# Performance work log

Measured on AMD Instinct MI355X. Metric: run time of the kernel, lower is better.

## Reference

```python
import jax, jax.numpy as jnp
import numpy as np

WS = 6        # window size -> N = 36 tokens per window
HEADS = 16

def _rel_index(ws):
    coords = np.stack(np.meshgrid(np.arange(ws), np.arange(ws), indexing='ij')).reshape(2, -1)
    rel = coords[:, :, None] - coords[:, None, :] + (ws - 1)
    return jnp.asarray(rel[0] * (2 * ws - 1) + rel[1])  # (N, N) int

REL_IDX = _rel_index(WS)

def _ln(x, g, b, eps=1e-5):
    m = x.mean(-1, keepdims=True)
    v = x.var(-1, keepdims=True)
    return (x - m) / jnp.sqrt(v + eps) * g + b

def setup_inputs() -> dict:
    key = jax.random.key(0)
    ks = jax.random.split(key, 6)
    B, H, W, C = 16, 96, 96, 512
    hid = 4 * C
    s = 0.02
    return {
        'x': jax.random.normal(ks[0], (B, H, W, C), jnp.float32),
        'w_qkv': jax.random.normal(ks[1], (C, 3 * C), jnp.float32) * s,
        'w_proj': jax.random.normal(ks[2], (C, C), jnp.float32) * s,
        'b_proj': jnp.zeros((C,), jnp.float32),
        'rel_bias': jax.random.normal(ks[3], ((2 * WS - 1) ** 2, HEADS), jnp.float32) * s,
        'ln1_g': jnp.ones((C,), jnp.float32), 'ln1_b': jnp.zeros((C,), jnp.float32),
        'ln2_g': jnp.ones((C,), jnp.float32), 'ln2_b': jnp.zeros((C,), jnp.float32),
        'w_fc1': jax.random.normal(ks[4], (C, hid), jnp.float32) * s,
        'b_fc1': jnp.zeros((hid,), jnp.float32),
        'w_fc2': jax.random.normal(ks[5], (hid, C), jnp.float32) * s,
        'b_fc2': jnp.zeros((C,), jnp.float32),
    }

def reference(x, w_qkv, w_proj, b_proj, rel_bias, ln1_g, ln1_b, ln2_g, ln2_b, w_fc1, b_fc1, w_fc2, b_fc2):
    B, H, W, C = x.shape
    h, d, N = HEADS, C // HEADS, WS * WS
    nh, nw = H // WS, W // WS
    # window partition: (B,H,W,C) -> (B*nh*nw, N, C)
    xw = x.reshape(B, nh, WS, nw, WS, C).transpose(0, 1, 3, 2, 4, 5).reshape(B * nh * nw, N, C)
    xn = _ln(xw, ln1_g, ln1_b)
    qkv = xn @ w_qkv
    q, k, v = jnp.split(qkv, 3, axis=-1)
    to_heads = lambda t: t.reshape(-1, N, h, d).transpose(0, 2, 1, 3)  # (B_, h, N, d)
    q = to_heads(q) * (d ** -0.5)
    k = to_heads(k)
    v = to_heads(v)
    attn = jnp.einsum('bhnd,bhmd->bhnm', q, k)
    bias = rel_bias[REL_IDX.reshape(-1)].reshape(N, N, h).transpose(2, 0, 1)  # (h, N, N)
    attn = jax.nn.softmax(attn + bias[None], axis=-1)
    o = jnp.einsum('bhnm,bhmd->bhnd', attn, v).transpose(0, 2, 1, 3).reshape(-1, N, C)
    o = o @ w_proj + b_proj
    # un-window; NOTE: source has no residual around attention (x is replaced)
    x2 = o.reshape(B, nh, nw, WS, WS, C).transpose(0, 1, 3, 2, 4, 5).reshape(B, H, W, C)
    xm = _ln(x2, ln2_g, ln2_b)
    mlp = jax.nn.gelu(xm @ w_fc1 + b_fc1, approximate=False) @ w_fc2 + b_fc2
    return x2 + mlp
```

## Files before the change

kernel.cpp:

```cpp
#include <hip/hip_runtime.h>
#include <stdint.h>

#define TOK 147456
#define CCH 512

typedef __attribute__((ext_vector_type(8))) short short8;
typedef __attribute__((ext_vector_type(4))) float f32x4;

struct alignas(8) US4 { unsigned short a, b, c, d; };

typedef __attribute__((address_space(3))) void lds_void;
typedef const __attribute__((address_space(1))) void gbl_void;

__device__ inline void gload16(const void* g, void* l) {
    __builtin_amdgcn_global_load_lds((gbl_void*)g, (lds_void*)l, 16, 0, 0);
}

__device__ inline unsigned short f2bf(float f) {
    union { float f; unsigned u; } v{f};
    unsigned r = v.u + 0x7fffu + ((v.u >> 16) & 1u);
    return (unsigned short)(r >> 16);
}
__device__ inline float bf2f(unsigned short h) {
    union { unsigned u; float f; } v; v.u = ((unsigned)h) << 16; return v.f;
}
__device__ inline float frcp(float x) {
    float r; asm("v_rcp_f32 %0, %1" : "=v"(r) : "v"(x)); return r;
}

__global__ void wprep(const float* __restrict__ in, unsigned short* __restrict__ out,
                      int K, int N) {
    int idx = blockIdx.x * 256 + threadIdx.x;
    if (idx >= K * N) return;
    int k = idx / N, n = idx % N;
    out[(size_t)n * K + k] = f2bf(in[idx]);
}

__global__ void biasprep(const float* __restrict__ rb, float* __restrict__ bb) {
    int idx = blockIdx.x * 256 + threadIdx.x;
    if (idx >= 16 * 48 * 48) return;
    int h = idx / 2304, rem = idx % 2304, r = rem / 48, c = rem % 48;
    float v = -1e9f;
    if (r < 36 && c < 36) {
        int dy = r / 6 - c / 6 + 5;
        int dx = r % 6 - c % 6 + 5;
        v = rb[(dy * 11 + dx) * 16 + h];
    }
    bb[idx] = v;
}

__global__ __launch_bounds__(256) void ln_k(const float* __restrict__ x,
                                            const float* __restrict__ g,
                                            const float* __restrict__ b,
                                            unsigned short* __restrict__ out, int ntok) {
    int lane = threadIdx.x & 63;
    int tok = blockIdx.x * 4 + (threadIdx.x >> 6);
    if (tok >= ntok) return;
    const float4* xr = (const float4*)(x + (size_t)tok * CCH);
    float4 v0 = xr[lane], v1 = xr[lane + 64];
    float s  = v0.x + v0.y + v0.z + v0.w + v1.x + v1.y + v1.z + v1.w;
    float s2 = v0.x*v0.x + v0.y*v0.y + v0.z*v0.z + v0.w*v0.w
             + v1.x*v1.x + v1.y*v1.y + v1.z*v1.z + v1.w*v1.w;
#pragma unroll
    for (int off = 32; off; off >>= 1) { s += __shfl_xor(s, off); s2 += __shfl_xor(s2, off); }
    float mean = s * (1.f / 512.f);
    float var  = s2 * (1.f / 512.f) - mean * mean;
    float inv  = rsqrtf(var + 1e-5f);
    const float4* gp = (const float4*)g;
    const float4* bp = (const float4*)b;
    float4 g0 = gp[lane], g1 = gp[lane + 64], b0 = bp[lane], b1 = bp[lane + 64];
    US4 o0, o1;
    o0.a = f2bf((v0.x - mean) * inv * g0.x + b0.x);
    o0.b = f2bf((v0.y - mean) * inv * g0.y + b0.y);
    o0.c = f2bf((v0.z - mean) * inv * g0.z + b0.z);
    o0.d = f2bf((v0.w - mean) * inv * g0.w + b0.w);
    o1.a = f2bf((v1.x - mean) * inv * g1.x + b1.x);
    o1.b = f2bf((v1.y - mean) * inv * g1.y + b1.y);
    o1.c = f2bf((v1.z - mean) * inv * g1.z + b1.z);
    o1.d = f2bf((v1.w - mean) * inv * g1.w + b1.w);
    unsigned short* op = out + (size_t)tok * CCH;
    *(US4*)(op + 4 * lane)       = o0;
    *(US4*)(op + 256 + 4 * lane) = o1;
}

__global__ __launch_bounds__(256) void ln_bf(const unsigned short* __restrict__ x,
                                             const float* __restrict__ g,
                                             const float* __restrict__ b,
                                             unsigned short* __restrict__ out, int ntok) {
    int lane = threadIdx.x & 63;
    int tok = blockIdx.x * 4 + (threadIdx.x >> 6);
    if (tok >= ntok) return;
    short8 v = *(const short8*)(x + (size_t)tok * CCH + lane * 8);
    float f[8];
#pragma unroll
    for (int j = 0; j < 8; ++j) f[j] = bf2f((unsigned short)v[j]);
    float s = 0.f, s2 = 0.f;
#pragma unroll
    for (int j = 0; j < 8; ++j) { s += f[j]; s2 += f[j] * f[j]; }
#pragma unroll
    for (int off = 32; off; off >>= 1) { s += __shfl_xor(s, off); s2 += __shfl_xor(s2, off); }
    float mean = s * (1.f / 512.f);
    float var  = s2 * (1.f / 512.f) - mean * mean;
    float inv  = rsqrtf(var + 1e-5f);
    const float4* gp = (const float4*)g + lane * 2;
    const float4* bp = (const float4*)b + lane * 2;
    float4 g0 = gp[0], g1 = gp[1], b0 = bp[0], b1 = bp[1];
    float gg[8] = {g0.x, g0.y, g0.z, g0.w, g1.x, g1.y, g1.z, g1.w};
    float bb[8] = {b0.x, b0.y, b0.z, b0.w, b1.x, b1.y, b1.z, b1.w};
    short8 o;
#pragma unroll
    for (int j = 0; j < 8; ++j) o[j] = (short)f2bf((f[j] - mean) * inv * gg[j] + bb[j]);
    *(short8*)(out + (size_t)tok * CCH + lane * 8) = o;
}

__global__ __launch_bounds__(256) void attn_mfma(const unsigned short* __restrict__ qkv,
                                                 const float* __restrict__ biasb,
                                                 unsigned short* __restrict__ o) {
    __shared__ __align__(16) unsigned short p_lds[4][48 * 64];
    __shared__ __align__(16) unsigned short v_lds[4][32 * 64];

    int tid  = threadIdx.x;
    int wv   = tid >> 6;
    int lane = tid & 63;
    int l15  = lane & 15;
    int g    = lane >> 4;

    int wid = blockIdx.x * 4 + wv;
    int h   = wid & 15;
    int win = wid >> 4;
    int img  = win >> 8;
    int wrow = (win >> 4) & 15;
    int wcol = win & 15;
    int tok_base = (img * 96 + wrow * 6) * 96 + wcol * 6;

    unsigned short* pw = p_lds[wv];
    unsigned short* vw = v_lds[wv];

    #define TOKOF(r) (tok_base + (r) + 90 * ((r) / 6))

    short8 z8 = {};
    for (int e = lane; e < 224; e += 64) {
        if (e < 128) {
            int ch = e >> 2, kst = 32 + (e & 3) * 8;
            *(short8*)(vw + ch * 64 + (kst ^ ((ch & 7) << 3))) = z8;
        } else {
            int ee = e - 128; int q = ee >> 1, kst = 48 + (ee & 1) * 8;
            *(short8*)(pw + q * 64 + (kst ^ ((q & 7) << 3))) = z8;
        }
    }

    for (int e = lane; e < 144; e += 64) {
        int r = e >> 2, c0 = (e & 3) * 8;
        short8 vv = *(const short8*)(qkv + (size_t)TOKOF(r) * 1536 + 1024 + h * 32 + c0);
#pragma unroll
        for (int j = 0; j < 8; ++j) {
            int ch = c0 + j;
            vw[ch * 64 + (r ^ ((ch & 7) << 3))] = (unsigned short)vv[j];
        }
    }

    short8 qf[3], kf[3];
#pragma unroll
    for (int t = 0; t < 3; ++t) {
        int r = t * 16 + l15;
        if (r < 36) {
            size_t ba = (size_t)TOKOF(r) * 1536 + h * 32 + g * 8;
            qf[t] = *(const short8*)(qkv + ba);
            kf[t] = *(const short8*)(qkv + ba + 512);
        } else { qf[t] = z8; kf[t] = z8; }
    }

    f32x4 s[3][3] = {};
#pragma unroll
    for (int mt = 0; mt < 3; ++mt)
#pragma unroll
        for (int nt = 0; nt < 3; ++nt)
            s[mt][nt] = __builtin_amdgcn_mfma_f32_16x16x32_bf16(qf[mt], kf[nt], s[mt][nt], 0, 0, 0);

    const float SCALE = 0.17677669529663687f;
    const float* bh = biasb + h * 2304;
#pragma unroll
    for (int mt = 0; mt < 3; ++mt) {
#pragma unroll
        for (int r = 0; r < 4; ++r) {
            int row = mt * 16 + g * 4 + r;
            const float* bb = bh + row * 48 + l15;
            float v0 = fmaf(s[mt][0][r], SCALE, bb[0]);
            float v1 = fmaf(s[mt][1][r], SCALE, bb[16]);
            float v2 = fmaf(s[mt][2][r], SCALE, bb[32]);
            float m = fmaxf(fmaxf(v0, v1), v2);
#pragma unroll
            for (int off = 1; off < 16; off <<= 1) m = fmaxf(m, __shfl_xor(m, off));
            float e0 = __expf(v0 - m), e1 = __expf(v1 - m), e2 = __expf(v2 - m);
            float sm = e0 + e1 + e2;
#pragma unroll
            for (int off = 1; off < 16; off <<= 1) sm += __shfl_xor(sm, off);
            float inv = 1.f / sm;
            int sw = (row & 7) << 3;
            unsigned short* pr = pw + row * 64;
            pr[(l15)      ^ sw] = f2bf(e0 * inv);
            pr[(16 + l15) ^ sw] = f2bf(e1 * inv);
            pr[(32 + l15) ^ sw] = f2bf(e2 * inv);
        }
    }

    f32x4 oacc[3][2] = {};
#pragma unroll
    for (int ks = 0; ks < 2; ++ks) {
        int kst = ks * 32 + g * 8;
        short8 bfr[2];
#pragma unroll
        for (int nt = 0; nt < 2; ++nt) {
            int c = nt * 16 + l15;
            bfr[nt] = *(const short8*)(vw + c * 64 + (kst ^ ((c & 7) << 3)));
        }
#pragma unroll
        for (int mt = 0; mt < 3; ++mt) {
            int q = mt * 16 + l15;
            short8 pa = *(const short8*)(pw + q * 64 + (kst ^ ((q & 7) << 3)));
#pragma unroll
            for (int nt = 0; nt < 2; ++nt)
                oacc[mt][nt] = __builtin_amdgcn_mfma_f32_16x16x32_bf16(pa, bfr[nt], oacc[mt][nt], 0, 0, 0);
        }
    }

#pragma unroll
    for (int mt = 0; mt < 3; ++mt) {
#pragma unroll
        for (int r = 0; r < 4; ++r) {
            int q = mt * 16 + g * 4 + r;
            if (q < 36) {
                size_t rb = (size_t)TOKOF(q) * 512 + h * 32;
#pragma unroll
                for (int nt = 0; nt < 2; ++nt)
                    o[rb + nt * 16 + l15] = f2bf(oacc[mt][nt][r]);
            }
        }
    }
    #undef TOKOF
}

template <int EPI>
__global__ __launch_bounds__(512, 1) void gemm8(const unsigned short* __restrict__ A,
                                                const unsigned short* __restrict__ Bt,
                                                int M, int N, int K,
                                                const float* __restrict__ bias,
                                                const unsigned short* __restrict__ resid,
                                                void* __restrict__ Cout) {
    extern __shared__ char lds[];
    int tid = threadIdx.x;
    int w = tid >> 6, lane = tid & 63;
    int l15 = lane & 15, grp = lane >> 4, l7 = l15 & 7;
    int wm = w >> 2, wn = w & 3;

    int nbn = N >> 8;
    int nwg = gridDim.x;
    int q = nwg >> 3, r = nwg & 7;
    int xcd = blockIdx.x & 7, pos_ = blockIdx.x >> 3;
    int wgid = (xcd < r ? xcd * (q + 1) : r * (q + 1) + (xcd - r) * q) + pos_;
    int bm = wgid / nbn, bn = wgid % nbn;

    int NI = K >> 7;

    int trow = tid >> 3;
    int sg = (tid & 7) ^ (trow & 7);
    const unsigned short* aBase = A  + ((size_t)bm * 256 + trow) * (size_t)K + sg * 8;
    const unsigned short* bBase = Bt + ((size_t)bn * 256 + trow) * (size_t)K + sg * 8;

    #define STG(base, rowOff, kt, dst) do { \
        gload16((base) + (size_t)(rowOff) * K + (kt),        lds + (dst) + tid * 16); \
        gload16((base) + (size_t)((rowOff) + 64) * K + (kt), lds + (dst) + 8192 + tid * 16); } while (0)

    int aR0 = wm * 16384 + l15 * 128 + ((grp ^ l7) << 4);
    int bR0 = 32768 + (wn >> 1) * 16384 + (wn & 1) * 8192 + l15 * 128 + ((grp ^ l7) << 4);

    f32x4 acc[8][4] = {};
    short8 Af[4][2], Bf[4][2];

    STG(bBase, 0,   0,  32768);
    STG(bBase, 128, 0,  32768 + 16384);
    STG(aBase, 0,   0,  0);
    STG(aBase, 128, 0,  16384);
    STG(bBase, 0,   64, 65536 + 32768);
    STG(bBase, 128, 64, 65536 + 32768 + 16384);
    asm volatile("s_waitcnt vmcnt(4)" ::: "memory");
    __builtin_amdgcn_s_barrier();

    #define RDA(d, qm) do { int ab_ = (d) * 65536 + (qm) * 8192 + aR0; \
        _Pragma("unroll") for (int mi_ = 0; mi_ < 4; ++mi_) { \
            Af[mi_][0] = *(const short8*)(lds + ab_ + mi_ * 2048); \
            Af[mi_][1] = *(const short8*)(lds + ((ab_ + mi_ * 2048) ^ 64)); } } while (0)
    #define RDB(d, nh) do { int bb_ = (d) * 65536 + (nh) * 4096 + bR0; \
        _Pragma("unroll") for (int nj_ = 0; nj_ < 2; ++nj_) { \
            Bf[(nh) * 2 + nj_][0] = *(const short8*)(lds + bb_ + nj_ * 2048); \
            Bf[(nh) * 2 + nj_][1] = *(const short8*)(lds + ((bb_ + nj_ * 2048) ^ 64)); } } while (0)
    #define MFQ(qm, nh) do { \
        _Pragma("unroll") for (int mi_ = 0; mi_ < 4; ++mi_) \
        _Pragma("unroll") for (int nj_ = 0; nj_ < 2; ++nj_) \
        _Pragma("unroll") for (int ks_ = 0; ks_ < 2; ++ks_) \
            acc[(qm) * 4 + mi_][(nh) * 2 + nj_] = __builtin_amdgcn_mfma_f32_16x16x32_bf16( \
                Af[mi_][ks_], Bf[(nh) * 2 + nj_][ks_], acc[(qm) * 4 + mi_][(nh) * 2 + nj_], 0, 0, 0); } while (0)
    #define PH_PRE  do { __builtin_amdgcn_s_barrier(); \
        asm volatile("s_waitcnt lgkmcnt(0)" ::: "memory"); \
        __builtin_amdgcn_sched_barrier(0); \
        __builtin_amdgcn_s_setprio(1); } while (0)
    #define PH_POST do { __builtin_amdgcn_s_setprio(0); \
        __builtin_amdgcn_s_barrier(); } while (0)

    for (int i = 0; i < NI; ++i) {
        int tka = i << 7, tkb = tka + 64;
        bool pf = (i + 1 < NI);
        RDA(0, 0); RDB(0, 0);
        STG(aBase, 0, tkb, 65536);
        PH_PRE; MFQ(0, 0); PH_POST;
        RDB(0, 1);
        STG(aBase, 128, tkb, 65536 + 16384);
        PH_PRE; MFQ(0, 1); PH_POST;
        RDA(0, 1);
        if (pf) STG(bBase, 0, tka + 128, 32768);
        PH_PRE; MFQ(1, 0); PH_POST;
        if (pf) {
            STG(bBase, 128, tka + 128, 32768 + 16384);
            asm volatile("s_waitcnt vmcnt(4)" ::: "memory");
        } else {
            asm volatile("s_waitcnt vmcnt(0)" ::: "memory");
        }
        PH_PRE; MFQ(1, 1); PH_POST;
        RDA(1, 0); RDB(1, 0);
        if (pf) STG(aBase, 0, tka + 128, 0);
        PH_PRE; MFQ(0, 0); PH_POST;
        RDB(1, 1);
        if (pf) STG(aBase, 128, tka + 128, 16384);
        PH_PRE; MFQ(0, 1); PH_POST;
        RDA(1, 1);
        if (pf) STG(bBase, 0, tkb + 128, 65536 + 32768);
        PH_PRE; MFQ(1, 0); PH_POST;
        if (pf) {
            STG(bBase, 128, tkb + 128, 65536 + 32768 + 16384);
            asm volatile("s_waitcnt vmcnt(4)" ::: "memory");
        }
        PH_PRE; MFQ(1, 1); PH_POST;
    }
    #undef STG
    #undef RDA
    #undef RDB
    #undef MFQ
    #undef PH_PRE
    #undef PH_POST

    int row0 = bm * 256 + wm * 128 + grp * 4;
    int col0 = bn * 256 + wn * 64 + l15;
#pragma unroll
    for (int m = 0; m < 8; ++m) {
#pragma unroll
        for (int n = 0; n < 4; ++n) {
            int col = col0 + n * 16;
            float bv = (EPI == 0) ? 0.f : bias[col];
#pragma unroll
            for (int r2 = 0; r2 < 4; ++r2) {
                int row = row0 + m * 16 + r2;
                size_t idx = (size_t)row * N + col;
                float val = acc[m][n][r2] + bv;
                if (EPI == 0) {
                    ((unsigned short*)Cout)[idx] = f2bf(val);
                } else if (EPI == 1) {
                    ((unsigned short*)Cout)[idx] = f2bf(val);
                } else if (EPI == 2) {
                    float t1 = val * val;
                    float t2 = fmaf(t1, 0.0713548163f, 1.5957691216f);
                    float z  = val * t2;
                    float e  = __expf(z);
                    float rr = frcp(e + 1.f);
                    float ge = val - val * rr;
                    ((unsigned short*)Cout)[idx] = f2bf(ge);
                } else {
                    ((float*)Cout)[idx] = val + bf2f(resid[idx]);
                }
            }
        }
    }
}

extern "C" void kernel_launch(void* const* d_in, const int* in_sizes, int n_in,
                              void* d_out, int out_size, void* d_ws, size_t ws_size,
                              hipStream_t stream) {
    const float* x       = (const float*)d_in[0];
    const float* w_qkv   = (const float*)d_in[1];
    const float* w_proj  = (const float*)d_in[2];
    const float* b_proj  = (const float*)d_in[3];
    const float* relb    = (const float*)d_in[4];
    const float* ln1g    = (const float*)d_in[5];
    const float* ln1b    = (const float*)d_in[6];
    const float* ln2g    = (const float*)d_in[7];
    const float* ln2b    = (const float*)d_in[8];
    const float* w_fc1   = (const float*)d_in[9];
    const float* b_fc1   = (const float*)d_in[10];
    const float* w_fc2   = (const float*)d_in[11];
    const float* b_fc2   = (const float*)d_in[12];
    float* out = (float*)d_out;

    hipFuncSetAttribute(reinterpret_cast<const void*>(&gemm8<0>),
                        hipFuncAttributeMaxDynamicSharedMemorySize, 131072);
    hipFuncSetAttribute(reinterpret_cast<const void*>(&gemm8<1>),
                        hipFuncAttributeMaxDynamicSharedMemorySize, 131072);
    hipFuncSetAttribute(reinterpret_cast<const void*>(&gemm8<2>),
                        hipFuncAttributeMaxDynamicSharedMemorySize, 131072);
    hipFuncSetAttribute(reinterpret_cast<const void*>(&gemm8<3>),
                        hipFuncAttributeMaxDynamicSharedMemorySize, 131072);

    char* w = (char*)d_ws;
    unsigned short* wT_qkv  = (unsigned short*)w; w += (size_t)1536 * 512 * 2;
    unsigned short* wT_proj = (unsigned short*)w; w += (size_t)512  * 512 * 2;
    unsigned short* wT_fc1  = (unsigned short*)w; w += (size_t)2048 * 512 * 2;
    unsigned short* wT_fc2  = (unsigned short*)w; w += (size_t)512  * 2048 * 2;
    float* biasb            = (float*)w;          w += (size_t)16 * 48 * 48 * 4;
    size_t wbytes = (size_t)(w - (char*)d_ws);

    int nchunk = 16;
    for (int c = 1; c <= 16; c *= 2) {
        size_t tokc = TOK / c;
        if (wbytes + tokc * 6144 <= ws_size) { nchunk = c; break; }
    }
    size_t tokc = TOK / nchunk;
    unsigned short* buf1 = (unsigned short*)w;
    unsigned short* buf2 = (unsigned short*)(w + tokc * 1024);
    unsigned short* buf3 = (unsigned short*)(w + tokc * 5120);

    wprep<<<(512 * 1536 + 255) / 256, 256, 0, stream>>>(w_qkv,  wT_qkv,  512, 1536);
    wprep<<<(512 * 512  + 255) / 256, 256, 0, stream>>>(w_proj, wT_proj, 512, 512);
    wprep<<<(512 * 2048 + 255) / 256, 256, 0, stream>>>(w_fc1,  wT_fc1,  512, 2048);
    wprep<<<(2048 * 512 + 255) / 256, 256, 0, stream>>>(w_fc2,  wT_fc2,  2048, 512);
    biasprep<<<(16 * 48 * 48 + 255) / 256, 256, 0, stream>>>(relb, biasb);

    int Mc = (int)tokc;
    int gm = Mc / 256;
    int imgs = Mc / 9216;

    for (int c = 0; c < nchunk; ++c) {
        size_t toff = (size_t)c * tokc;
        const float* xc = x + toff * CCH;
        float* outc = out + toff * CCH;

        ln_k<<<Mc / 4, 256, 0, stream>>>(xc, ln1g, ln1b, buf1, Mc);
        gemm8<0><<<gm * 6, 512, 131072, stream>>>(buf1, wT_qkv, Mc, 1536, 512,
                                                  nullptr, nullptr, buf2);
        attn_mfma<<<imgs * 1024, 256, 0, stream>>>(buf2, biasb, buf1);
        gemm8<1><<<gm * 2, 512, 131072, stream>>>(buf1, wT_proj, Mc, 512, 512,
                                                  b_proj, nullptr, buf3);
        ln_bf<<<Mc / 4, 256, 0, stream>>>(buf3, ln2g, ln2b, buf1, Mc);
        gemm8<2><<<gm * 8, 512, 131072, stream>>>(buf1, wT_fc1, Mc, 2048, 512,
                                                  b_fc1, nullptr, buf2);
        gemm8<3><<<gm * 2, 512, 131072, stream>>>(buf2, wT_fc2, Mc, 512, 2048,
                                                  b_fc2, buf3, outc);
    }
}
```

Before: 1.508 ms.

## Make GEMM persistent with cross-tile prefetch and vectorized transposed epilogue

The GEMM becomes a persistent kernel with a fixed grid of 256 workgroups. Each workgroup loops over output tiles using the XCD-aware tile mapping and prefetches the next tile's first K-slices during the last K iteration of the current tile. The goal is to hide the pipeline prologue and tail between tiles and to avoid wave quantization. The MFMA operands are swapped so each lane holds four consecutive columns, which lets the epilogue write 4-wide vector stores and load bias and residual as vectors. The risks are more register pressure and the epilogue still serializing against the next tile's compute.

Result: slower. 1.590 ms (+5.5%).

```diff
diff --git a/kernel.cpp b/kernel.cpp
--- a/kernel.cpp
+++ b/kernel.cpp
@@ -254,18 +254,17 @@
     int wm = w >> 2, wn = w & 3;
 
     int nbn = N >> 8;
+    int ntiles = (M >> 8) * nbn;
+    int NI = K >> 7;
     int nwg = gridDim.x;
-    int q = nwg >> 3, r = nwg & 7;
-    int xcd = blockIdx.x & 7, pos_ = blockIdx.x >> 3;
-    int wgid = (xcd < r ? xcd * (q + 1) : r * (q + 1) + (xcd - r) * q) + pos_;
-    int bm = wgid / nbn, bn = wgid % nbn;
-
-    int NI = K >> 7;
+
+    int tq = ntiles >> 3, tr = ntiles & 7;
+    #define TMAP(t, bmv, bnv) do { int x_ = (t) & 7, p_ = (t) >> 3; \
+        int wg_ = (x_ < tr ? x_ * (tq + 1) : tr * (tq + 1) + (x_ - tr) * tq) + p_; \
+        bmv = wg_ / nbn; bnv = wg_ % nbn; } while (0)
 
     int trow = tid >> 3;
     int sg = (tid & 7) ^ (trow & 7);
-    const unsigned short* aBase = A  + ((size_t)bm * 256 + trow) * (size_t)K + sg * 8;
-    const unsigned short* bBase = Bt + ((size_t)bn * 256 + trow) * (size_t)K + sg * 8;
 
     #define STG(base, rowOff, kt, dst) do { \
         gload16((base) + (size_t)(rowOff) * K + (kt),        lds + (dst) + tid * 16); \
@@ -276,6 +275,11 @@
 
     f32x4 acc[8][4] = {};
     short8 Af[4][2], Bf[4][2];
+
+    int traw = blockIdx.x;
+    int bm, bn; TMAP(traw, bm, bn);
+    const unsigned short* aBase = A  + ((size_t)bm * 256 + trow) * (size_t)K + sg * 8;
+    const unsigned short* bBase = Bt + ((size_t)bn * 256 + trow) * (size_t)K + sg * 8;
 
     STG(bBase, 0,   0,  32768);
     STG(bBase, 128, 0,  32768 + 16384);
@@ -299,7 +303,7 @@
         _Pragma("unroll") for (int nj_ = 0; nj_ < 2; ++nj_) \
         _Pragma("unroll") for (int ks_ = 0; ks_ < 2; ++ks_) \
             acc[(qm) * 4 + mi_][(nh) * 2 + nj_] = __builtin_amdgcn_mfma_f32_16x16x32_bf16( \
-                Af[mi_][ks_], Bf[(nh) * 2 + nj_][ks_], acc[(qm) * 4 + mi_][(nh) * 2 + nj_], 0, 0, 0); } while (0)
+                Bf[(nh) * 2 + nj_][ks_], Af[mi_][ks_], acc[(qm) * 4 + mi_][(nh) * 2 + nj_], 0, 0, 0); } while (0)
     #define PH_PRE  do { __builtin_amdgcn_s_barrier(); \
         asm volatile("s_waitcnt lgkmcnt(0)" ::: "memory"); \
         __builtin_amdgcn_sched_barrier(0); \
@@ -307,39 +311,106 @@
     #define PH_POST do { __builtin_amdgcn_s_setprio(0); \
         __builtin_amdgcn_s_barrier(); } while (0)
 
-    for (int i = 0; i < NI; ++i) {
-        int tka = i << 7, tkb = tka + 64;
-        bool pf = (i + 1 < NI);
-        RDA(0, 0); RDB(0, 0);
-        STG(aBase, 0, tkb, 65536);
-        PH_PRE; MFQ(0, 0); PH_POST;
-        RDB(0, 1);
-        STG(aBase, 128, tkb, 65536 + 16384);
-        PH_PRE; MFQ(0, 1); PH_POST;
-        RDA(0, 1);
-        if (pf) STG(bBase, 0, tka + 128, 32768);
-        PH_PRE; MFQ(1, 0); PH_POST;
-        if (pf) {
-            STG(bBase, 128, tka + 128, 32768 + 16384);
-            asm volatile("s_waitcnt vmcnt(4)" ::: "memory");
-        } else {
-            asm volatile("s_waitcnt vmcnt(0)" ::: "memory");
-        }
-        PH_PRE; MFQ(1, 1); PH_POST;
-        RDA(1, 0); RDB(1, 0);
-        if (pf) STG(aBase, 0, tka + 128, 0);
-        PH_PRE; MFQ(0, 0); PH_POST;
-        RDB(1, 1);
-        if (pf) STG(aBase, 128, tka + 128, 16384);
-        PH_PRE; MFQ(0, 1); PH_POST;
-        RDA(1, 1);
-        if (pf) STG(bBase, 0, tkb + 128, 65536 + 32768);
-        PH_PRE; MFQ(1, 0); PH_POST;
-        if (pf) {
-            STG(bBase, 128, tkb + 128, 65536 + 32768 + 16384);
-            asm volatile("s_waitcnt vmcnt(4)" ::: "memory");
-        }
-        PH_PRE; MFQ(1, 1); PH_POST;
+    while (true) {
+        int tnext = traw + nwg;
+        bool hasNext = tnext < ntiles;
+        const unsigned short* aNB = aBase;
+        const unsigned short* bNB = bBase;
+        if (hasNext) {
+            int bm2, bn2; TMAP(tnext, bm2, bn2);
+            aNB = A  + ((size_t)bm2 * 256 + trow) * (size_t)K + sg * 8;
+            bNB = Bt + ((size_t)bn2 * 256 + trow) * (size_t)K + sg * 8;
+        }
+        for (int i = 0; i < NI; ++i) {
+            int tka = i << 7, tkb = tka + 64;
+            bool lastI = (i + 1 == NI);
+            const unsigned short* aS = lastI ? aNB : aBase;
+            const unsigned short* bS = lastI ? bNB : bBase;
+            int ktN = lastI ? 0 : (tka + 128);
+            bool pf = (!lastI) || hasNext;
+            RDA(0, 0); RDB(0, 0);
+            STG(aBase, 0, tkb, 65536);
+            PH_PRE; MFQ(0, 0); PH_POST;
+            RDB(0, 1);
+            STG(aBase, 128, tkb, 65536 + 16384);
+            PH_PRE; MFQ(0, 1); PH_POST;
+            RDA(0, 1);
+            if (pf) STG(bS, 0, ktN, 32768);
+            PH_PRE; MFQ(1, 0); PH_POST;
+            if (pf) {
+                STG(bS, 128, ktN, 32768 + 16384);
+                asm volatile("s_waitcnt vmcnt(4)" ::: "memory");
+            } else {
+                asm volatile("s_waitcnt vmcnt(0)" ::: "memory");
+            }
+            PH_PRE; MFQ(1, 1); PH_POST;
+            RDA(1, 0); RDB(1, 0);
+            if (pf) STG(aS, 0, ktN, 0);
+            PH_PRE; MFQ(0, 0); PH_POST;
+            RDB(1, 1);
+            if (pf) STG(aS, 128, ktN, 16384);
+            PH_PRE; MFQ(0, 1); PH_POST;
+            RDA(1, 1);
+            if (pf) STG(bS, 0, ktN + 64, 65536 + 32768);
+            PH_PRE; MFQ(1, 0); PH_POST;
+            if (pf) {
+                STG(bS, 128, ktN + 64, 65536 + 32768 + 16384);
+                asm volatile("s_waitcnt vmcnt(4)" ::: "memory");
+            }
+            PH_PRE; MFQ(1, 1); PH_POST;
+        }
+
+        {
+            int rowB = bm * 256 + wm * 128 + l15;
+            int colB = bn * 256 + wn * 64 + grp * 4;
+#pragma unroll
+            for (int mi = 0; mi < 8; ++mi) {
+                int row = rowB + mi * 16;
+#pragma unroll
+                for (int ni = 0; ni < 4; ++ni) {
+                    size_t base = (size_t)row * N + colB + ni * 16;
+                    f32x4 v = acc[mi][ni];
+                    float4 bv = {0.f, 0.f, 0.f, 0.f};
+                    if (EPI != 0) bv = *(const float4*)(bias + colB + ni * 16);
+                    float x0 = v[0] + bv.x, x1 = v[1] + bv.y, x2 = v[2] + bv.z, x3 = v[3] + bv.w;
+                    if (EPI == 0 || EPI == 1) {
+                        US4 o = {f2bf(x0), f2bf(x1), f2bf(x2), f2bf(x3)};
+                        *(US4*)((unsigned short*)Cout + base) = o;
+                    } else if (EPI == 2) {
+                        float xs[4] = {x0, x1, x2, x3};
+                        US4 o;
+                        unsigned short* op = &o.a;
+#pragma unroll
+                        for (int j = 0; j < 4; ++j) {
+                            float val = xs[j];
+                            float t1 = val * val;
+                            float t2 = fmaf(t1, 0.0713548163f, 1.5957691216f);
+                            float z  = val * t2;
+                            float e  = __expf(z);
+                            float rr = frcp(e + 1.f);
+                            op[j] = f2bf(val - val * rr);
+                        }
+                        *(US4*)((unsigned short*)Cout + base) = o;
+                    } else {
+                        US4 rv = *(const US4*)(resid + base);
+                        float4 o;
+                        o.x = x0 + bf2f(rv.a);
+                        o.y = x1 + bf2f(rv.b);
+                        o.z = x2 + bf2f(rv.c);
+                        o.w = x3 + bf2f(rv.d);
+                        *(float4*)((float*)Cout + base) = o;
+                    }
+                }
+            }
+        }
+
+        if (!hasNext) break;
+        traw = tnext; bm = 0; bn = 0; TMAP(traw, bm, bn);
+        aBase = aNB; bBase = bNB;
+#pragma unroll
+        for (int m = 0; m < 8; ++m)
+#pragma unroll
+            for (int n = 0; n < 4; ++n) acc[m][n] = (f32x4){0.f, 0.f, 0.f, 0.f};
     }
     #undef STG
     #undef RDA
@@ -347,38 +418,7 @@
     #undef MFQ
     #undef PH_PRE
     #undef PH_POST
-
-    int row0 = bm * 256 + wm * 128 + grp * 4;
-    int col0 = bn * 256 + wn * 64 + l15;
-#pragma unroll
-    for (int m = 0; m < 8; ++m) {
-#pragma unroll
-        for (int n = 0; n < 4; ++n) {
-            int col = col0 + n * 16;
-            float bv = (EPI == 0) ? 0.f : bias[col];
-#pragma unroll
-            for (int r2 = 0; r2 < 4; ++r2) {
-                int row = row0 + m * 16 + r2;
-                size_t idx = (size_t)row * N + col;
-                float val = acc[m][n][r2] + bv;
-                if (EPI == 0) {
-                    ((unsigned short*)Cout)[idx] = f2bf(val);
-                } else if (EPI == 1) {
-                    ((unsigned short*)Cout)[idx] = f2bf(val);
-                } else if (EPI == 2) {
-                    float t1 = val * val;
-                    float t2 = fmaf(t1, 0.0713548163f, 1.5957691216f);
-                    float z  = val * t2;
-                    float e  = __expf(z);
-                    float rr = frcp(e + 1.f);
-                    float ge = val - val * rr;
-                    ((unsigned short*)Cout)[idx] = f2bf(ge);
-                } else {
-                    ((float*)Cout)[idx] = val + bf2f(resid[idx]);
-                }
-            }
-        }
-    }
+    #undef TMAP
 }
 
 extern "C" void kernel_launch(void* const* d_in, const int* in_sizes, int n_in,
@@ -433,8 +473,8 @@
     biasprep<<<(16 * 48 * 48 + 255) / 256, 256, 0, stream>>>(relb, biasb);
 
     int Mc = (int)tokc;
-    int gm = Mc / 256;
     int imgs = Mc / 9216;
+    const int PGRID = 256;
 
     for (int c = 0; c < nchunk; ++c) {
         size_t toff = (size_t)c * tokc;
@@ -442,15 +482,15 @@
         float* outc = out + toff * CCH;
 
         ln_k<<<Mc / 4, 256, 0, stream>>>(xc, ln1g, ln1b, buf1, Mc);
-        gemm8<0><<<gm * 6, 512, 131072, stream>>>(buf1, wT_qkv, Mc, 1536, 512,
-                                                  nullptr, nullptr, buf2);
+        gemm8<0><<<PGRID, 512, 131072, stream>>>(buf1, wT_qkv, Mc, 1536, 512,
+                                                 nullptr, nullptr, buf2);
         attn_mfma<<<imgs * 1024, 256, 0, stream>>>(buf2, biasb, buf1);
-        gemm8<1><<<gm * 2, 512, 131072, stream>>>(buf1, wT_proj, Mc, 512, 512,
-                                                  b_proj, nullptr, buf3);
+        gemm8<1><<<PGRID, 512, 131072, stream>>>(buf1, wT_proj, Mc, 512, 512,
+                                                 b_proj, nullptr, buf3);
         ln_bf<<<Mc / 4, 256, 0, stream>>>(buf3, ln2g, ln2b, buf1, Mc);
-        gemm8<2><<<gm * 8, 512, 131072, stream>>>(buf1, wT_fc1, Mc, 2048, 512,
-                                                  b_fc1, nullptr, buf2);
-        gemm8<3><<<gm * 2, 512, 131072, stream>>>(buf2, wT_fc2, Mc, 512, 2048,
-                                                  b_fc2, buf3, outc);
-    }
-}
+        gemm8<2><<<PGRID, 512, 131072, stream>>>(buf1, wT_fc1, Mc, 2048, 512,
+                                                 b_fc1, nullptr, buf2);
+        gemm8<3><<<PGRID, 512, 131072, stream>>>(buf2, wT_fc2, Mc, 512, 2048,
+                                                 b_fc2, buf3, outc);
+    }
+}
```
